# Optimization experiments

Hardware: AMD Instinct MI355X
Metric: run time of the kernel (lower is better)

## Reference

```python
import jax, jax.numpy as jnp
import numpy as np

B, V, J, P = 1024, 5023, 5, 36
PARENTS = np.array([0, 0, 1, 1, 1], dtype=np.int64)  # FLAME kinematic chain


def setup_inputs() -> dict:
    key = jax.random.key(0)
    ks = jax.random.split(key, 8)
    return {
        "v_shaped_expressed": jax.random.normal(ks[0], (B, V, 3), jnp.float32) * 0.1,
        "global_pose_params_6d": jax.random.normal(ks[1], (B, 6), jnp.float32),
        "neck_pose_params_ax": jax.random.normal(ks[2], (B, 3), jnp.float32) * 0.1,
        "jaw_pose_params_ax": jax.random.normal(ks[3], (B, 3), jnp.float32) * 0.1,
        "eye_pose_params_ax": jax.random.normal(ks[4], (B, 6), jnp.float32) * 0.1,
        "J_transformed_rest": jax.random.normal(ks[5], (B, J, 3), jnp.float32) * 0.1,
        "lbs_weights": jax.nn.softmax(jax.random.normal(ks[6], (V, J), jnp.float32), axis=-1),
        "posedirs": jax.random.normal(ks[7], (V, P, 3), jnp.float32) * 0.01,
        "parents": jnp.asarray(PARENTS),
    }


def batch_rodrigues(rv, eps=1e-8):
    # rv: [B,3] axis-angle -> [B,3,3] rotation matrices
    angle = jnp.linalg.norm(rv + eps, axis=1, keepdims=True)  # [B,1]
    d = rv / angle
    cos = jnp.cos(angle)[:, :, None]
    sin = jnp.sin(angle)[:, :, None]
    rx, ry, rz = d[:, 0], d[:, 1], d[:, 2]
    z = jnp.zeros_like(rx)
    K = jnp.stack([z, -rz, ry, rz, z, -rx, -ry, rx, z], axis=1).reshape(-1, 3, 3)
    I = jnp.eye(3, dtype=rv.dtype)[None]
    return I + sin * K + (1.0 - cos) * (K @ K)


def rot6d_to_matrix(x):
    # Zhou et al. 6D rotation -> [B,3,3] (rows b1,b2,b3, as pytorch3d)
    a1, a2 = x[:, :3], x[:, 3:]
    b1 = a1 / jnp.linalg.norm(a1, axis=-1, keepdims=True)
    b2 = a2 - jnp.sum(b1 * a2, axis=-1, keepdims=True) * b1
    b2 = b2 / jnp.linalg.norm(b2, axis=-1, keepdims=True)
    b3 = jnp.cross(b1, b2)
    return jnp.stack([b1, b2, b3], axis=-2)


def make_T(R, t):
    # R [...,3,3], t [...,3] -> homogeneous [...,4,4]
    top = jnp.concatenate([R, t[..., None]], axis=-1)
    bot = jnp.broadcast_to(jnp.array([0.0, 0.0, 0.0, 1.0], R.dtype), top.shape[:-2] + (1, 4))
    return jnp.concatenate([top, bot], axis=-2)


def batch_rigid_transform(rot_mats, joints, parents):
    # rot_mats [B,J,3,3], joints [B,J,3]; parents: numpy int array (constant)
    rel = joints.at[:, 1:].add(-joints[:, parents[1:]])
    Tm = make_T(rot_mats, rel)  # [B,J,4,4]
    chain = [Tm[:, 0]]
    for i in range(1, parents.shape[0]):  # tiny fixed chain (J=5)
        chain.append(chain[int(parents[i])] @ Tm[:, i])
    tr = jnp.stack(chain, axis=1)  # [B,J,4,4]
    posed_joints = tr[:, :, :3, 3]
    R = tr[:, :, :3, :3]
    t = posed_joints - jnp.einsum('bjhw,bjw->bjh', R, joints)
    return posed_joints, make_T(R, t)


def reference(v_shaped_expressed, global_pose_params_6d, neck_pose_params_ax,
              jaw_pose_params_ax, eye_pose_params_ax, J_transformed_rest,
              lbs_weights, posedirs, parents):
    parents = np.asarray(parents)
    Rg = rot6d_to_matrix(global_pose_params_6d)
    Rn = batch_rodrigues(neck_pose_params_ax)
    Rj = batch_rodrigues(jaw_pose_params_ax)
    Rel = batch_rodrigues(eye_pose_params_ax[:, :3])
    Rer = batch_rodrigues(eye_pose_params_ax[:, 3:])
    rot_mats = jnp.stack([Rg, Rn, Rj, Rel, Rer], axis=1)  # [B,5,3,3]

    _, A = batch_rigid_transform(rot_mats, J_transformed_rest, parents)  # [B,5,4,4]

    # pose blendshapes from joints 1..4 (neck/jaw/eyes): [B, 36]
    b = rot_mats.shape[0]
    pose_feat = (rot_mats[:, 1:5] - jnp.eye(3, dtype=rot_mats.dtype)).reshape(b, -1)
    pose_bs = jnp.einsum('bp,vpc->bvc', pose_feat, posedirs)
    v = v_shaped_expressed + pose_bs  # [B,V,3]

    # linear blend skinning
    T = jnp.einsum('vj,bjhw->bvhw', lbs_weights, A)  # [B,V,4,4]
    v_h = jnp.concatenate([v, jnp.ones(v.shape[:2] + (1,), v.dtype)], axis=-1)
    v_posed = jnp.einsum('bvhw,bvw->bvh', T, v_h)[:, :, :3]
    return v_posed
```

## Files before the change

### kernel.cpp

```cpp
#include <hip/hip_runtime.h>
#include <math.h>

constexpr int Bn = 1024, Vn = 5023;
constexpr int NB = 32;
constexpr int PARAM_STRIDE = 96;


__device__ inline void rodrigues3(float rx, float ry, float rz, float R[9]) {
    const float eps = 1e-8f;
    float ax = rx + eps, ay = ry + eps, az = rz + eps;
    float ang = sqrtf(ax * ax + ay * ay + az * az);
    float inv = 1.0f / ang;
    float dx = rx * inv, dy = ry * inv, dz = rz * inv;
    float s = sinf(ang), c = cosf(ang), omc = 1.0f - c;
    float K[9] = {0.f, -dz, dy, dz, 0.f, -dx, -dy, dx, 0.f};
    float K2[9];
#pragma unroll
    for (int r = 0; r < 3; r++)
#pragma unroll
        for (int k = 0; k < 3; k++) {
            float acc = 0.f;
#pragma unroll
            for (int i = 0; i < 3; i++) acc += K[r * 3 + i] * K[i * 3 + k];
            K2[r * 3 + k] = acc;
        }
#pragma unroll
    for (int i = 0; i < 9; i++) R[i] = s * K[i] + omc * K2[i];
    R[0] += 1.f; R[4] += 1.f; R[8] += 1.f;
}

__device__ inline void rot6d(const float* x, float R[9]) {
    float a1x = x[0], a1y = x[1], a1z = x[2];
    float a2x = x[3], a2y = x[4], a2z = x[5];
    float n1 = sqrtf(a1x * a1x + a1y * a1y + a1z * a1z);
    float b1x = a1x / n1, b1y = a1y / n1, b1z = a1z / n1;
    float d = b1x * a2x + b1y * a2y + b1z * a2z;
    float tx = a2x - d * b1x, ty = a2y - d * b1y, tz = a2z - d * b1z;
    float n2 = sqrtf(tx * tx + ty * ty + tz * tz);
    float b2x = tx / n2, b2y = ty / n2, b2z = tz / n2;
    float b3x = b1y * b2z - b1z * b2y;
    float b3y = b1z * b2x - b1x * b2z;
    float b3z = b1x * b2y - b1y * b2x;
    R[0] = b1x; R[1] = b1y; R[2] = b1z;
    R[3] = b2x; R[4] = b2y; R[5] = b2z;
    R[6] = b3x; R[7] = b3y; R[8] = b3z;
}

__device__ inline void compose(const float* Rp, const float* tp,
                               const float* Ri, const float* ti,
                               float* Ro, float* to) {
#pragma unroll
    for (int r = 0; r < 3; r++) {
#pragma unroll
        for (int c = 0; c < 3; c++) {
            Ro[r * 3 + c] = Rp[r * 3 + 0] * Ri[0 * 3 + c] +
                            Rp[r * 3 + 1] * Ri[1 * 3 + c] +
                            Rp[r * 3 + 2] * Ri[2 * 3 + c];
        }
        to[r] = Rp[r * 3 + 0] * ti[0] + Rp[r * 3 + 1] * ti[1] +
                Rp[r * 3 + 2] * ti[2] + tp[r];
    }
}

__global__ void flame_params_kernel(const float* __restrict__ g6,
                                    const float* __restrict__ neck,
                                    const float* __restrict__ jaw,
                                    const float* __restrict__ eye,
                                    const float* __restrict__ jrest,
                                    float* __restrict__ params) {
    int b = blockIdx.x * blockDim.x + threadIdx.x;
    if (b >= Bn) return;

    float R[5][9];
    rot6d(g6 + b * 6, R[0]);
    rodrigues3(neck[b * 3 + 0], neck[b * 3 + 1], neck[b * 3 + 2], R[1]);
    rodrigues3(jaw[b * 3 + 0], jaw[b * 3 + 1], jaw[b * 3 + 2], R[2]);
    rodrigues3(eye[b * 6 + 0], eye[b * 6 + 1], eye[b * 6 + 2], R[3]);
    rodrigues3(eye[b * 6 + 3], eye[b * 6 + 4], eye[b * 6 + 5], R[4]);

    float j[5][3];
#pragma unroll
    for (int i = 0; i < 5; i++) {
        j[i][0] = jrest[b * 15 + i * 3 + 0];
        j[i][1] = jrest[b * 15 + i * 3 + 1];
        j[i][2] = jrest[b * 15 + i * 3 + 2];
    }
    float rel[5][3];
#pragma unroll
    for (int c = 0; c < 3; c++) {
        rel[0][c] = j[0][c];
        rel[1][c] = j[1][c] - j[0][c];
        rel[2][c] = j[2][c] - j[1][c];
        rel[3][c] = j[3][c] - j[1][c];
        rel[4][c] = j[4][c] - j[1][c];
    }

    float CR[5][9], CT[5][3];
#pragma unroll
    for (int i = 0; i < 9; i++) CR[0][i] = R[0][i];
#pragma unroll
    for (int c = 0; c < 3; c++) CT[0][c] = rel[0][c];
    compose(CR[0], CT[0], R[1], rel[1], CR[1], CT[1]);
    compose(CR[1], CT[1], R[2], rel[2], CR[2], CT[2]);
    compose(CR[1], CT[1], R[3], rel[3], CR[3], CT[3]);
    compose(CR[1], CT[1], R[4], rel[4], CR[4], CT[4]);

    float* P = params + b * PARAM_STRIDE;
#pragma unroll
    for (int jj = 0; jj < 4; jj++)
#pragma unroll
        for (int r = 0; r < 3; r++)
#pragma unroll
            for (int c = 0; c < 3; c++)
                P[jj * 9 + r * 3 + c] = R[jj + 1][r * 3 + c] - (r == c ? 1.f : 0.f);
#pragma unroll
    for (int i = 0; i < 5; i++) {
#pragma unroll
        for (int r = 0; r < 3; r++) {
            float t = CT[i][r] - (CR[i][r * 3 + 0] * j[i][0] +
                                  CR[i][r * 3 + 1] * j[i][1] +
                                  CR[i][r * 3 + 2] * j[i][2]);
            P[36 + i * 12 + r * 4 + 0] = CR[i][r * 3 + 0];
            P[36 + i * 12 + r * 4 + 1] = CR[i][r * 3 + 1];
            P[36 + i * 12 + r * 4 + 2] = CR[i][r * 3 + 2];
            P[36 + i * 12 + r * 4 + 3] = t;
        }
    }
}

__global__ __launch_bounds__(256) void flame_main_kernel(
    const float* __restrict__ vsh, const float* __restrict__ lbs,
    const float* __restrict__ pdirs, const float* __restrict__ params,
    float* __restrict__ out) {
    int v = blockIdx.x * 256 + threadIdx.x;
    bool valid = v < Vn;
    int vc = valid ? v : (Vn - 1);

    float pd[108];
#pragma unroll
    for (int i = 0; i < 27; i++) {
        float4 t = *reinterpret_cast<const float4*>(pdirs + (size_t)vc * 108 + i * 4);
        pd[i * 4 + 0] = t.x;
        pd[i * 4 + 1] = t.y;
        pd[i * 4 + 2] = t.z;
        pd[i * 4 + 3] = t.w;
    }
    float w[5];
#pragma unroll
    for (int jj = 0; jj < 5; jj++) w[jj] = lbs[(size_t)vc * 5 + jj];

    int b0 = blockIdx.y * NB;
    for (int bi = 0; bi < NB; bi++) {
        int b = b0 + bi;
        const float* __restrict__ P = params + b * PARAM_STRIDE;

        float ax = 0.f, ay = 0.f, az = 0.f;
#pragma unroll
        for (int p = 0; p < 36; p++) {
            float f = P[p];
            ax = fmaf(f, pd[p * 3 + 0], ax);
            ay = fmaf(f, pd[p * 3 + 1], ay);
            az = fmaf(f, pd[p * 3 + 2], az);
        }

        size_t base = ((size_t)b * Vn + vc) * 3;
        float x = vsh[base + 0] + ax;
        float y = vsh[base + 1] + ay;
        float z = vsh[base + 2] + az;

        float ox = 0.f, oy = 0.f, oz = 0.f;
#pragma unroll
        for (int jj = 0; jj < 5; jj++) {
            const float* Aj = P + 36 + jj * 12;
            float wj = w[jj];
            float rx = fmaf(Aj[0], x, fmaf(Aj[1], y, fmaf(Aj[2], z, Aj[3])));
            float ry = fmaf(Aj[4], x, fmaf(Aj[5], y, fmaf(Aj[6], z, Aj[7])));
            float rz = fmaf(Aj[8], x, fmaf(Aj[9], y, fmaf(Aj[10], z, Aj[11])));
            ox = fmaf(wj, rx, ox);
            oy = fmaf(wj, ry, oy);
            oz = fmaf(wj, rz, oz);
        }
        if (valid) {
            out[base + 0] = ox;
            out[base + 1] = oy;
            out[base + 2] = oz;
        }
    }
}

extern "C" void kernel_launch(void* const* d_in, const int* in_sizes, int n_in,
                              void* d_out, int out_size, void* d_ws, size_t ws_size,
                              hipStream_t stream) {
    const float* vsh   = (const float*)d_in[0];
    const float* g6    = (const float*)d_in[1];
    const float* neck  = (const float*)d_in[2];
    const float* jaw   = (const float*)d_in[3];
    const float* eye   = (const float*)d_in[4];
    const float* jrest = (const float*)d_in[5];
    const float* lbs   = (const float*)d_in[6];
    const float* pdirs = (const float*)d_in[7];
    float* out = (float*)d_out;
    float* params = (float*)d_ws;

    hipLaunchKernelGGL(flame_params_kernel, dim3((Bn + 255) / 256), dim3(256), 0,
                       stream, g6, neck, jaw, eye, jrest, params);

    dim3 grid((Vn + 255) / 256, Bn / NB);
    hipLaunchKernelGGL(flame_main_kernel, grid, dim3(256), 0, stream, vsh, lbs,
                       pdirs, params, out);
}
```

Before: 59.47 us.

## Stage posedirs as bf16 in LDS and process two batches per iteration

The 108-float posedirs cache per vertex moves out of registers into shared memory, packed as bf16 pairs, so register pressure drops and occupancy can rise (launch bounds now ask for 4 blocks). Each block covers 128 vertices with two 128-thread halves handling separate batch halves. Each thread processes two batches per loop iteration with float4 param loads, and the grid is reshaped with NB=16. Rounding posedirs to bf16 adds numerical error to the pose blendshape term, which could matter for tolerance.

```diff
diff --git a/kernel.cpp b/kernel.cpp
--- a/kernel.cpp
+++ b/kernel.cpp
@@ -2,7 +2,7 @@
 #include <math.h>
 
 constexpr int Bn = 1024, Vn = 5023;
-constexpr int NB = 32;
+constexpr int NB = 16;
 constexpr int PARAM_STRIDE = 96;
 
 
@@ -128,62 +128,119 @@
     }
 }
 
-__global__ __launch_bounds__(256) void flame_main_kernel(
+
+__device__ inline uint32_t pack_bf2(float a, float b) {
+    uint32_t ua = __float_as_uint(a);
+    uint32_t ub = __float_as_uint(b);
+    uint32_t ra = (ua + 0x7FFFu + ((ua >> 16) & 1u)) >> 16;
+    uint32_t rb = (ub + 0x7FFFu + ((ub >> 16) & 1u)) >> 16;
+    return (ra & 0xFFFFu) | (rb << 16);
+}
+__device__ inline float blo(uint32_t d) { return __uint_as_float(d << 16); }
+__device__ inline float bhi(uint32_t d) { return __uint_as_float(d); }
+
+__global__ __launch_bounds__(256, 4) void flame_main_kernel(
     const float* __restrict__ vsh, const float* __restrict__ lbs,
     const float* __restrict__ pdirs, const float* __restrict__ params,
     float* __restrict__ out) {
-    int v = blockIdx.x * 256 + threadIdx.x;
-    bool valid = v < Vn;
-    int vc = valid ? v : (Vn - 1);
-
-    float pd[108];
-#pragma unroll
-    for (int i = 0; i < 27; i++) {
-        float4 t = *reinterpret_cast<const float4*>(pdirs + (size_t)vc * 108 + i * 4);
-        pd[i * 4 + 0] = t.x;
-        pd[i * 4 + 1] = t.y;
-        pd[i * 4 + 2] = t.z;
-        pd[i * 4 + 3] = t.w;
-    }
-    float w[5];
-#pragma unroll
-    for (int jj = 0; jj < 5; jj++) w[jj] = lbs[(size_t)vc * 5 + jj];
-
-    int b0 = blockIdx.y * NB;
-    for (int bi = 0; bi < NB; bi++) {
-        int b = b0 + bi;
-        const float* __restrict__ P = params + b * PARAM_STRIDE;
-
-        float ax = 0.f, ay = 0.f, az = 0.f;
-#pragma unroll
-        for (int p = 0; p < 36; p++) {
-            float f = P[p];
-            ax = fmaf(f, pd[p * 3 + 0], ax);
-            ay = fmaf(f, pd[p * 3 + 1], ay);
-            az = fmaf(f, pd[p * 3 + 2], az);
-        }
-
-        size_t base = ((size_t)b * Vn + vc) * 3;
-        float x = vsh[base + 0] + ax;
-        float y = vsh[base + 1] + ay;
-        float z = vsh[base + 2] + az;
-
-        float ox = 0.f, oy = 0.f, oz = 0.f;
+    const int tid = threadIdx.x;
+    const int vt = tid & 127;
+    const int bh = tid >> 7;
+    const int v = blockIdx.x * 128 + vt;
+    const bool valid = v < Vn;
+    const int vc = valid ? v : (Vn - 1);
+    const int bstart = blockIdx.y * NB + bh * (NB / 2);
+
+    __shared__ uint32_t shd[128 * 54];
+
+    {
+        const size_t g0 = (size_t)blockIdx.x * 128 * 108;
+        const size_t gmax = (size_t)Vn * 108 - 2;
+#pragma unroll
+        for (int i = 0; i < 27; i++) {
+            int p = i * 256 + tid;
+            size_t g = g0 + (size_t)p * 2;
+            if (g > gmax) g = gmax;
+            float2 f = *reinterpret_cast<const float2*>(pdirs + g);
+            shd[p] = pack_bf2(f.x, f.y);
+        }
+    }
+    __syncthreads();
+
+    float wgt[5];
+#pragma unroll
+    for (int jj = 0; jj < 5; jj++) wgt[jj] = lbs[(size_t)vc * 5 + jj];
+
+    const uint2* __restrict__ my =
+        reinterpret_cast<const uint2*>(shd + vt * 54);
+
+#pragma unroll 1
+    for (int pr = 0; pr < NB / 4; pr++) {
+        const int bA = bstart + pr * 2;
+        const int bB = bA + 1;
+        const float4* __restrict__ PA =
+            reinterpret_cast<const float4*>(params + (size_t)bA * PARAM_STRIDE);
+        const float4* __restrict__ PB =
+            reinterpret_cast<const float4*>(params + (size_t)bB * PARAM_STRIDE);
+        const size_t baseA = ((size_t)bA * Vn + vc) * 3;
+        const size_t baseB = ((size_t)bB * Vn + vc) * 3;
+
+        float axA = vsh[baseA + 0], ayA = vsh[baseA + 1], azA = vsh[baseA + 2];
+        float axB = vsh[baseB + 0], ayB = vsh[baseB + 1], azB = vsh[baseB + 2];
+
+#pragma unroll
+        for (int g = 0; g < 9; g++) {
+            float4 fA = PA[g];
+            float4 fB = PB[g];
+            uint2 c0 = my[3 * g + 0];
+            uint2 c1 = my[3 * g + 1];
+            uint2 c2 = my[3 * g + 2];
+            float p0 = blo(c0.x), p1 = bhi(c0.x), p2 = blo(c0.y);
+            float p3 = bhi(c0.y), p4 = blo(c1.x), p5 = bhi(c1.x);
+            float p6 = blo(c1.y), p7 = bhi(c1.y), p8 = blo(c2.x);
+            float p9 = bhi(c2.x), p10 = blo(c2.y), p11 = bhi(c2.y);
+
+            axA = fmaf(fA.x, p0, axA); ayA = fmaf(fA.x, p1, ayA); azA = fmaf(fA.x, p2, azA);
+            axB = fmaf(fB.x, p0, axB); ayB = fmaf(fB.x, p1, ayB); azB = fmaf(fB.x, p2, azB);
+            axA = fmaf(fA.y, p3, axA); ayA = fmaf(fA.y, p4, ayA); azA = fmaf(fA.y, p5, azA);
+            axB = fmaf(fB.y, p3, axB); ayB = fmaf(fB.y, p4, ayB); azB = fmaf(fB.y, p5, azB);
+            axA = fmaf(fA.z, p6, axA); ayA = fmaf(fA.z, p7, ayA); azA = fmaf(fA.z, p8, azA);
+            axB = fmaf(fB.z, p6, axB); ayB = fmaf(fB.z, p7, ayB); azB = fmaf(fB.z, p8, azB);
+            axA = fmaf(fA.w, p9, axA); ayA = fmaf(fA.w, p10, ayA); azA = fmaf(fA.w, p11, azA);
+            axB = fmaf(fB.w, p9, axB); ayB = fmaf(fB.w, p10, ayB); azB = fmaf(fB.w, p11, azB);
+        }
+
+        float oxA = 0.f, oyA = 0.f, ozA = 0.f;
+        float oxB = 0.f, oyB = 0.f, ozB = 0.f;
 #pragma unroll
         for (int jj = 0; jj < 5; jj++) {
-            const float* Aj = P + 36 + jj * 12;
-            float wj = w[jj];
-            float rx = fmaf(Aj[0], x, fmaf(Aj[1], y, fmaf(Aj[2], z, Aj[3])));
-            float ry = fmaf(Aj[4], x, fmaf(Aj[5], y, fmaf(Aj[6], z, Aj[7])));
-            float rz = fmaf(Aj[8], x, fmaf(Aj[9], y, fmaf(Aj[10], z, Aj[11])));
-            ox = fmaf(wj, rx, ox);
-            oy = fmaf(wj, ry, oy);
-            oz = fmaf(wj, rz, oz);
+            float wj = wgt[jj];
+            float4 r0 = PA[9 + jj * 3 + 0];
+            float4 r1 = PA[9 + jj * 3 + 1];
+            float4 r2 = PA[9 + jj * 3 + 2];
+            float rx = fmaf(r0.x, axA, fmaf(r0.y, ayA, fmaf(r0.z, azA, r0.w)));
+            float ry = fmaf(r1.x, axA, fmaf(r1.y, ayA, fmaf(r1.z, azA, r1.w)));
+            float rz = fmaf(r2.x, axA, fmaf(r2.y, ayA, fmaf(r2.z, azA, r2.w)));
+            oxA = fmaf(wj, rx, oxA);
+            oyA = fmaf(wj, ry, oyA);
+            ozA = fmaf(wj, rz, ozA);
+            float4 s0 = PB[9 + jj * 3 + 0];
+            float4 s1 = PB[9 + jj * 3 + 1];
+            float4 s2 = PB[9 + jj * 3 + 2];
+            float sx = fmaf(s0.x, axB, fmaf(s0.y, ayB, fmaf(s0.z, azB, s0.w)));
+            float sy = fmaf(s1.x, axB, fmaf(s1.y, ayB, fmaf(s1.z, azB, s1.w)));
+            float sz = fmaf(s2.x, axB, fmaf(s2.y, ayB, fmaf(s2.z, azB, s2.w)));
+            oxB = fmaf(wj, sx, oxB);
+            oyB = fmaf(wj, sy, oyB);
+            ozB = fmaf(wj, sz, ozB);
         }
         if (valid) {
-            out[base + 0] = ox;
-            out[base + 1] = oy;
-            out[base + 2] = oz;
+            out[baseA + 0] = oxA;
+            out[baseA + 1] = oyA;
+            out[baseA + 2] = ozA;
+            out[baseB + 0] = oxB;
+            out[baseB + 1] = oyB;
+            out[baseB + 2] = ozB;
         }
     }
 }
@@ -205,7 +262,7 @@
     hipLaunchKernelGGL(flame_params_kernel, dim3((Bn + 255) / 256), dim3(256), 0,
                        stream, g6, neck, jaw, eye, jrest, params);
 
-    dim3 grid((Vn + 255) / 256, Bn / NB);
+    dim3 grid((Vn + 127) / 128, Bn / NB);
     hipLaunchKernelGGL(flame_main_kernel, grid, dim3(256), 0, stream, vsh, lbs,
                        pdirs, params, out);
 }
```

Measured after the change: 82.17 us. 38.2% more time.
